# Kernel optimization log

Hardware: AMD Instinct MI355X
Metric: run time of the kernel (lower is better)

Reference implementation:

```python
import jax, jax.numpy as jnp
import numpy as np

D_MODEL = 320
N_CH = 129
N_TIMES = 200
D_STATE = 32
HEADDIM = 32
D_CONV = 4
N_LAYERS = 4
N_HEADS = 16
EPS = 1e-5


def _ln(x, w, b):
    m = jnp.mean(x, -1, keepdims=True)
    v = jnp.var(x, -1, keepdims=True)
    return (x - m) / jnp.sqrt(v + EPS) * w + b


def _mha(x, wqkv, bqkv, wo, bo, h):
    # torch nn.MultiheadAttention (batch_first, eval mode, avg attn weights)
    B, L, D = x.shape
    hd = D // h
    qkv = x @ wqkv.T + bqkv
    q, k, v = jnp.split(qkv, 3, axis=-1)
    sp = lambda t: t.reshape(B, L, h, hd).transpose(0, 2, 1, 3)
    q, k, v = sp(q), sp(k), sp(v)
    attn = jax.nn.softmax(jnp.einsum('bhqd,bhkd->bhqk', q, k) / np.sqrt(hd).astype(np.float32), axis=-1)
    o = jnp.einsum('bhqk,bhkd->bhqd', attn, v).transpose(0, 2, 1, 3).reshape(B, L, D)
    return o @ wo.T + bo, attn.mean(axis=1)


def _mamba2(u, in_w, conv_w, conv_b, dt_bias, A_log, Dskip, gn_w, out_w):
    # Mamba2 block, reference (non-fused) path, ngroups=1
    B, L, D = u.shape
    din = 2 * D
    H = din // HEADDIM
    P, N = HEADDIM, D_STATE
    zxbcdt = u @ in_w.T                       # (B,L,2*din+2N+H)
    z = zxbcdt[..., :din]
    xBC = zxbcdt[..., din:2 * din + 2 * N]
    dt = jax.nn.softplus(zxbcdt[..., -H:] + dt_bias)   # (B,L,H)
    # causal depthwise conv1d, kernel D_CONV, then silu
    xp = jnp.pad(xBC, ((0, 0), (D_CONV - 1, 0), (0, 0)))
    xc = conv_b + sum(xp[:, k:k + L, :] * conv_w[:, k] for k in range(D_CONV))
    xc = xc * jax.nn.sigmoid(xc)
    xh = xc[..., :din].reshape(B, L, H, P)
    Bm = xc[..., din:din + N]                 # (B,L,N)
    Cm = xc[..., din + N:]                    # (B,L,N)
    dA = jnp.exp(dt * (-jnp.exp(A_log)))      # (B,L,H)

    def step(st, inp):
        dA_t, dt_t, x_t, B_t, C_t = inp
        st = st * dA_t[:, :, None, None] + jnp.einsum('bh,bhp,bn->bhpn', dt_t, x_t, B_t)
        return st, jnp.einsum('bhpn,bn->bhp', st, C_t)

    mv = lambda t: jnp.moveaxis(t, 1, 0)
    st0 = jnp.zeros((B, H, P, N), u.dtype)
    _, ys = jax.lax.scan(step, st0, (mv(dA), mv(dt), mv(xh), mv(Bm), mv(Cm)))
    y = jnp.moveaxis(ys, 0, 1) + Dskip[None, None, :, None] * xh   # (B,L,H,P)
    y = y.reshape(B, L, din) * (z * jax.nn.sigmoid(z))             # gate
    y = y * jax.lax.rsqrt(jnp.mean(y * y, -1, keepdims=True) + EPS) * gn_w
    return y @ out_w.T


def _forward(x, sp_conv_w, sp_conv_b, sp_qkv_w, sp_qkv_b, sp_out_w, sp_out_b,
             sp_ln1_w, sp_ln1_b, sp_ff1_w, sp_ff1_b, sp_ff2_w, sp_ff2_b,
             sp_ln2_w, sp_ln2_b, norm_in_w, norm_in_b,
             m_in_w, m_conv_w, m_conv_b, m_dt_bias, m_A_log, m_D, m_gnorm_w, m_out_w,
             ln_w, ln_b, pm_qkv_w, pm_qkv_b, pm_out_w, pm_out_b, pm_ln_w, pm_ln_b,
             pool_w1, pool_b1, pool_w2, pool_b2, head_w1, head_b1, head_w2, head_b2):
    # spatial encoder: 1x1 conv projection -> MHA -> FFN
    h = jnp.einsum('bcl,dc->bld', x, sp_conv_w) + sp_conv_b        # (B,L,D)
    ha, sp_attn = _mha(h, sp_qkv_w, sp_qkv_b, sp_out_w, sp_out_b, N_HEADS)
    h = _ln(h + ha, sp_ln1_w, sp_ln1_b)
    ff = jax.nn.gelu(h @ sp_ff1_w.T + sp_ff1_b, approximate=False) @ sp_ff2_w.T + sp_ff2_b
    h = _ln(h + ff, sp_ln2_w, sp_ln2_b)
    h = _ln(h, norm_in_w, norm_in_b)
    # stacked pre-norm Mamba2 blocks with residuals
    for i in range(N_LAYERS):
        res = h
        h = _ln(h, ln_w[i], ln_b[i])
        h = _mamba2(h, m_in_w[i], m_conv_w[i], m_conv_b[i], m_dt_bias[i],
                    m_A_log[i], m_D[i], m_gnorm_w[i], m_out_w[i])
        h = h + res
    ha, post_attn = _mha(h, pm_qkv_w, pm_qkv_b, pm_out_w, pm_out_b, N_HEADS)
    h = _ln(h + ha, pm_ln_w, pm_ln_b)
    # attention-weighted pooling
    a = jnp.tanh(h @ pool_w1.T + pool_b1) @ pool_w2.T + pool_b2    # (B,L,1)
    a = jax.nn.softmax(a, axis=1)
    pooled = jnp.sum(h * a, axis=1)                                # (B,D)
    hr = jax.nn.gelu(pooled @ head_w1.T + head_b1, approximate=False)
    out = hr @ head_w2.T + head_b2                                 # (B,1)
    return out, sp_attn, post_attn, a.squeeze(-1)


def setup_inputs() -> dict:
    key = jax.random.key(0)
    ks = iter(jax.random.split(key, 64))
    nrm = lambda shape, s=0.02: jax.random.normal(next(ks), shape, jnp.float32) * s
    d, C, L, B = D_MODEL, N_CH, N_TIMES, 128
    din = 2 * d
    Hm = din // HEADDIM                       # 20 SSM heads
    dproj = 2 * din + 2 * D_STATE + Hm        # 1364
    cdim = din + 2 * D_STATE                  # 704
    nl = N_LAYERS
    return {
        'x': jax.random.normal(next(ks), (B, C, L), jnp.float32),
        'sp_conv_w': nrm((d, C)), 'sp_conv_b': jnp.zeros((d,), jnp.float32),
        'sp_qkv_w': nrm((3 * d, d)), 'sp_qkv_b': jnp.zeros((3 * d,), jnp.float32),
        'sp_out_w': nrm((d, d)), 'sp_out_b': jnp.zeros((d,), jnp.float32),
        'sp_ln1_w': jnp.ones((d,), jnp.float32), 'sp_ln1_b': jnp.zeros((d,), jnp.float32),
        'sp_ff1_w': nrm((2 * d, d)), 'sp_ff1_b': jnp.zeros((2 * d,), jnp.float32),
        'sp_ff2_w': nrm((d, 2 * d)), 'sp_ff2_b': jnp.zeros((d,), jnp.float32),
        'sp_ln2_w': jnp.ones((d,), jnp.float32), 'sp_ln2_b': jnp.zeros((d,), jnp.float32),
        'norm_in_w': jnp.ones((d,), jnp.float32), 'norm_in_b': jnp.zeros((d,), jnp.float32),
        'm_in_w': nrm((nl, dproj, d)),
        'm_conv_w': nrm((nl, cdim, D_CONV), 0.2),
        'm_conv_b': jnp.zeros((nl, cdim), jnp.float32),
        'm_dt_bias': jax.random.uniform(next(ks), (nl, Hm), jnp.float32, -0.1, 0.1),
        'm_A_log': jnp.log(jax.random.uniform(next(ks), (nl, Hm), jnp.float32, 1.0, 16.0)),
        'm_D': jnp.ones((nl, Hm), jnp.float32),
        'm_gnorm_w': jnp.ones((nl, din), jnp.float32),
        'm_out_w': nrm((nl, d, din)),
        'ln_w': jnp.ones((nl, d), jnp.float32), 'ln_b': jnp.zeros((nl, d), jnp.float32),
        'pm_qkv_w': nrm((3 * d, d)), 'pm_qkv_b': jnp.zeros((3 * d,), jnp.float32),
        'pm_out_w': nrm((d, d)), 'pm_out_b': jnp.zeros((d,), jnp.float32),
        'pm_ln_w': jnp.ones((d,), jnp.float32), 'pm_ln_b': jnp.zeros((d,), jnp.float32),
        'pool_w1': nrm((d // 4, d)), 'pool_b1': jnp.zeros((d // 4,), jnp.float32),
        'pool_w2': nrm((1, d // 4)), 'pool_b2': jnp.zeros((1,), jnp.float32),
        'head_w1': nrm((d // 2, d)), 'head_b1': jnp.zeros((d // 2,), jnp.float32),
        'head_w2': nrm((1, d // 2)), 'head_b2': jnp.zeros((1,), jnp.float32),
    }


def reference(x, sp_conv_w, sp_conv_b, sp_qkv_w, sp_qkv_b, sp_out_w, sp_out_b,
              sp_ln1_w, sp_ln1_b, sp_ff1_w, sp_ff1_b, sp_ff2_w, sp_ff2_b,
              sp_ln2_w, sp_ln2_b, norm_in_w, norm_in_b,
              m_in_w, m_conv_w, m_conv_b, m_dt_bias, m_A_log, m_D, m_gnorm_w, m_out_w,
              ln_w, ln_b, pm_qkv_w, pm_qkv_b, pm_out_w, pm_out_b, pm_ln_w, pm_ln_b,
              pool_w1, pool_b1, pool_w2, pool_b2, head_w1, head_b1, head_w2, head_b2):
    return _forward(x, sp_conv_w, sp_conv_b, sp_qkv_w, sp_qkv_b, sp_out_w, sp_out_b,
                    sp_ln1_w, sp_ln1_b, sp_ff1_w, sp_ff1_b, sp_ff2_w, sp_ff2_b,
                    sp_ln2_w, sp_ln2_b, norm_in_w, norm_in_b,
                    m_in_w, m_conv_w, m_conv_b, m_dt_bias, m_A_log, m_D, m_gnorm_w, m_out_w,
                    ln_w, ln_b, pm_qkv_w, pm_qkv_b, pm_out_w, pm_out_b, pm_ln_w, pm_ln_b,
                    pool_w1, pool_b1, pool_w2, pool_b2, head_w1, head_b1, head_w2, head_b2)
```

## Files before the change

kernel.cpp:

```cpp
#include <hip/hip_runtime.h>
#include <math.h>

#define BB 128
#define LL 200
#define DM 320
#define RTOT (BB*LL)
#define NCH 129
#define DIN 640
#define HM 20
#define PP 32
#define NN 32
#define CDIM 704
#define DPROJ 1364
#define NH 16
#define HD 20
#define ATTN_SCALE 0.22360679774997896f
#define KCONV 160

#define CH 32
#define NCHUNK 4
#define RC (CH*LL)

typedef unsigned short ushort;
typedef __attribute__((ext_vector_type(8))) short v8s;
typedef __attribute__((ext_vector_type(4))) float v4f;

static __device__ __forceinline__ float sigmoidf_(float x){ return 1.f/(1.f+__expf(-x)); }
static __device__ __forceinline__ float geluf_(float x){ return 0.5f*x*(1.f+erff(x*0.70710678118654752f)); }
static __device__ __forceinline__ ushort f2bf(float f){
  unsigned u = __float_as_uint(f);
  u = (u + 0x7FFFu + ((u>>16)&1u)) >> 16;
  return (ushort)u;
}
static __device__ __forceinline__ float bf2f(ushort h){ return __uint_as_float(((unsigned)h)<<16); }
static __device__ __forceinline__ void split3(float v, ushort* h, ushort* m, ushort* l){
  ushort hh = f2bf(v);
  float r1 = v - bf2f(hh);
  ushort mm = f2bf(r1);
  float r2 = r1 - bf2f(mm);
  *h = hh; *m = mm; *l = f2bf(r2);
}

static __device__ __forceinline__ float dpp_add_xor1(float v){
  return v + __int_as_float(__builtin_amdgcn_mov_dpp(__float_as_int(v), 0xB1, 0xF, 0xF, true));
}
static __device__ __forceinline__ float dpp_add_xor2(float v){
  return v + __int_as_float(__builtin_amdgcn_mov_dpp(__float_as_int(v), 0x4E, 0xF, 0xF, true));
}
static __device__ __forceinline__ float dpp_add_hm(float v){
  return v + __int_as_float(__builtin_amdgcn_mov_dpp(__float_as_int(v), 0x141, 0xF, 0xF, true));
}

#define GLL(g, s) __builtin_amdgcn_global_load_lds( \
    (const __attribute__((address_space(1))) unsigned int*)(g), \
    (__attribute__((address_space(3))) unsigned int*)(s), 16, 0, 0)

__global__ __launch_bounds__(256) void k_mgemm(
    const ushort* __restrict__ AH, const ushort* __restrict__ AM, const ushort* __restrict__ AL,
    const ushort* __restrict__ WH, const ushort* __restrict__ WM, const ushort* __restrict__ WL,
    const float* __restrict__ bias,
    float* __restrict__ outF, ushort* __restrict__ outH, ushort* __restrict__ outM, ushort* __restrict__ outL,
    int M, int N, int K, int lda, int act, int accum){
  __shared__ ushort sA0[128*32];
  __shared__ ushort sA1[128*32];
  __shared__ ushort sA2[128*32];
  __shared__ ushort sW0[128*32];
  __shared__ ushort sW1[128*32];
  __shared__ ushort sW2[128*32];
  int tid = threadIdx.x;
  int wid = tid>>6, lane = tid&63;
  int quad = lane>>4, col = lane&15;
  int m0 = blockIdx.y*128, n0 = blockIdx.x*128;
  int wm = (wid&1)*64, wn = (wid>>1)*64;
  v4f acc[4][4];
  #pragma unroll
  for (int i=0;i<4;i++)
    #pragma unroll
    for (int j=0;j<4;j++) acc[i][j] = (v4f)(0.f);

  int rl = lane>>2, kc8 = (lane&3)<<3;
  size_t aoff0 = (size_t)(m0 + 32*wid + rl)*lda + kc8;
  size_t aoff1 = aoff0 + (size_t)16*lda;
  int wr0 = n0 + 32*wid + rl;      if (wr0 > N-1) wr0 = N-1;
  int wr1 = n0 + 32*wid + 16 + rl; if (wr1 > N-1) wr1 = N-1;
  size_t woff0 = (size_t)wr0*K + kc8;
  size_t woff1 = (size_t)wr1*K + kc8;
  int sb0 = wid*1024, sb1 = wid*1024 + 512;

  for (int kb = 0; kb < K; kb += 32) {
    GLL(AH+aoff0+kb, &sA0[sb0]); GLL(AH+aoff1+kb, &sA0[sb1]);
    GLL(AM+aoff0+kb, &sA1[sb0]); GLL(AM+aoff1+kb, &sA1[sb1]);
    GLL(AL+aoff0+kb, &sA2[sb0]); GLL(AL+aoff1+kb, &sA2[sb1]);
    GLL(WH+woff0+kb, &sW0[sb0]); GLL(WH+woff1+kb, &sW0[sb1]);
    GLL(WM+woff0+kb, &sW1[sb0]); GLL(WM+woff1+kb, &sW1[sb1]);
    GLL(WL+woff0+kb, &sW2[sb0]); GLL(WL+woff1+kb, &sW2[sb1]);
    __syncthreads();
    v8s af[3][4];
    #pragma unroll
    for (int i=0;i<4;i++){
      int ro = (wm+16*i+col)*32 + quad*8;
      af[0][i] = *(const v8s*)&sA0[ro];
      af[1][i] = *(const v8s*)&sA1[ro];
      af[2][i] = *(const v8s*)&sA2[ro];
    }
    #pragma unroll
    for (int j=0;j<4;j++){
      int ro = (wn+16*j+col)*32 + quad*8;
      v8s b0 = *(const v8s*)&sW0[ro];
      v8s b1 = *(const v8s*)&sW1[ro];
      v8s b2 = *(const v8s*)&sW2[ro];
      #pragma unroll
      for (int i=0;i<4;i++){
        acc[i][j] = __builtin_amdgcn_mfma_f32_16x16x32_bf16(af[2][i], b0, acc[i][j], 0,0,0);
        acc[i][j] = __builtin_amdgcn_mfma_f32_16x16x32_bf16(af[1][i], b1, acc[i][j], 0,0,0);
        acc[i][j] = __builtin_amdgcn_mfma_f32_16x16x32_bf16(af[0][i], b2, acc[i][j], 0,0,0);
        acc[i][j] = __builtin_amdgcn_mfma_f32_16x16x32_bf16(af[1][i], b0, acc[i][j], 0,0,0);
        acc[i][j] = __builtin_amdgcn_mfma_f32_16x16x32_bf16(af[0][i], b1, acc[i][j], 0,0,0);
        acc[i][j] = __builtin_amdgcn_mfma_f32_16x16x32_bf16(af[0][i], b0, acc[i][j], 0,0,0);
      }
    }
    __syncthreads();
  }
  #pragma unroll
  for (int i=0;i<4;i++){
    int mb = m0 + wm + 16*i + quad*4;
    #pragma unroll
    for (int j=0;j<4;j++){
      int n = n0 + wn + 16*j + col;
      if (n >= N) continue;
      float bv = bias ? bias[n] : 0.f;
      #pragma unroll
      for (int r=0;r<4;r++){
        float v = acc[i][j][r] + bv;
        if (act == 1) v = geluf_(v);
        else if (act == 2) v = tanhf(v);
        size_t off = (size_t)(mb+r)*N + n;
        if (accum) v += outF[off];
        if (outF) outF[off] = v;
        if (outH) split3(v, outH+off, outM+off, outL+off);
      }
    }
  }
}

#define BM 128
#define BN 64
#define BKK 16
__global__ __launch_bounds__(256) void k_gemm(const float* __restrict__ A, const float* __restrict__ W,
    const float* __restrict__ bias, float* __restrict__ C, int M, int N, int K, int act, int accum){
  __shared__ float As[BKK][BM+4];
  __shared__ float Ws[BKK][BN+4];
  int tid = threadIdx.x;
  int m0 = blockIdx.y*BM, n0 = blockIdx.x*BN;
  int tx = tid & 15, ty = tid >> 4;
  float acc[8][4];
  #pragma unroll
  for (int i=0;i<8;i++)
    #pragma unroll
    for (int j=0;j<4;j++) acc[i][j]=0.f;
  for (int k0 = 0; k0 < K; k0 += BKK) {
    int r = tid >> 2, c4 = (tid & 3) << 2;
    #pragma unroll
    for (int hfl = 0; hfl < 2; hfl++) {
      int rr = r + hfl*64;
      float4 v = make_float4(0.f,0.f,0.f,0.f);
      if (m0 + rr < M && k0 + c4 < K)
        v = *(const float4*)(A + (size_t)(m0+rr)*K + k0 + c4);
      As[c4+0][rr]=v.x; As[c4+1][rr]=v.y; As[c4+2][rr]=v.z; As[c4+3][rr]=v.w;
    }
    {
      int n = tid >> 2;
      float4 v = make_float4(0.f,0.f,0.f,0.f);
      if (n0 + n < N && k0 + c4 < K)
        v = *(const float4*)(W + (size_t)(n0+n)*K + k0 + c4);
      Ws[c4+0][n]=v.x; Ws[c4+1][n]=v.y; Ws[c4+2][n]=v.z; Ws[c4+3][n]=v.w;
    }
    __syncthreads();
    #pragma unroll
    for (int kk = 0; kk < BKK; kk++) {
      float af[8], bf[4];
      float4 a0 = *(const float4*)&As[kk][ty*8];
      float4 a1 = *(const float4*)&As[kk][ty*8+4];
      af[0]=a0.x; af[1]=a0.y; af[2]=a0.z; af[3]=a0.w;
      af[4]=a1.x; af[5]=a1.y; af[6]=a1.z; af[7]=a1.w;
      float4 b0 = *(const float4*)&Ws[kk][tx*4];
      bf[0]=b0.x; bf[1]=b0.y; bf[2]=b0.z; bf[3]=b0.w;
      #pragma unroll
      for (int i=0;i<8;i++)
        #pragma unroll
        for (int j=0;j<4;j++) acc[i][j] = fmaf(af[i], bf[j], acc[i][j]);
    }
    __syncthreads();
  }
  #pragma unroll
  for (int i=0;i<8;i++){
    int m = m0 + ty*8 + i;
    if (m >= M) continue;
    #pragma unroll
    for (int j=0;j<4;j++){
      int n = n0 + tx*4 + j;
      if (n >= N) continue;
      float v = acc[i][j];
      if (bias) v += bias[n];
      if (act == 1) v = geluf_(v);
      else if (act == 2) v = tanhf(v);
      size_t off = (size_t)m*N + n;
      if (accum) v += C[off];
      C[off] = v;
    }
  }
}

__global__ __launch_bounds__(256) void k_wsplit(const float* __restrict__ src, ushort* __restrict__ hi,
    ushort* __restrict__ mi, ushort* __restrict__ lo, int N, int K, int Kp){
  int idx = blockIdx.x*256 + threadIdx.x;
  if (idx >= N*Kp) return;
  int n = idx / Kp, k = idx - n*Kp;
  float v = (k < K) ? src[(size_t)n*K + k] : 0.f;
  split3(v, hi+idx, mi+idx, lo+idx);
}

__global__ __launch_bounds__(256) void k_split(const float* __restrict__ src, ushort* __restrict__ hi,
    ushort* __restrict__ mi, ushort* __restrict__ lo, int n){
  int idx = blockIdx.x*256 + threadIdx.x;
  if (idx >= n) return;
  split3(src[idx], hi+idx, mi+idx, lo+idx);
}

__global__ __launch_bounds__(256) void k_tsplit(const float* __restrict__ x, ushort* __restrict__ hi,
    ushort* __restrict__ mi, ushort* __restrict__ lo, int r0g){
  int idx = blockIdx.x*256 + threadIdx.x;
  if (idx >= RC*KCONV) return;
  int r = idx / KCONV, c = idx - r*KCONV;
  int gr = r0g + r;
  int b = gr / LL, l = gr - b*LL;
  float v = (c < NCH) ? x[((size_t)b*NCH + c)*LL + l] : 0.f;
  split3(v, hi+idx, mi+idx, lo+idx);
}

__global__ __launch_bounds__(256) void k_ln(const float* __restrict__ A, const float* __restrict__ Badd,
    float* __restrict__ Of, ushort* __restrict__ Oh, ushort* __restrict__ Om, ushort* __restrict__ Ol,
    const float* __restrict__ w, const float* __restrict__ b, int nrows){
  int wid = threadIdx.x >> 6, lane = threadIdx.x & 63;
  int row = blockIdx.x*4 + wid;
  if (row >= nrows) return;
  const float* a = A + (size_t)row*DM;
  float x[5]; float s = 0.f;
  #pragma unroll
  for (int j=0;j<5;j++){
    int c = lane + j*64;
    x[j] = a[c];
    if (Badd) x[j] += Badd[(size_t)row*DM + c];
    s += x[j];
  }
  #pragma unroll
  for (int m=1;m<64;m<<=1) s += __shfl_xor(s, m);
  float mean = s * (1.f/DM);
  float vs = 0.f;
  #pragma unroll
  for (int j=0;j<5;j++){ float d = x[j]-mean; vs += d*d; }
  #pragma unroll
  for (int m=1;m<64;m<<=1) vs += __shfl_xor(vs, m);
  float inv = rsqrtf(vs*(1.f/DM) + 1e-5f);
  #pragma unroll
  for (int j=0;j<5;j++){
    int c = lane + j*64;
    float v = (x[j]-mean)*inv*w[c] + b[c];
    size_t off = (size_t)row*DM + c;
    if (Of) Of[off] = v;
    if (Oh) split3(v, Oh+off, Om+off, Ol+off);
  }
}

__global__ __launch_bounds__(256) void k_ln2x(const float* __restrict__ A, const float* __restrict__ F,
    const float* __restrict__ w2, const float* __restrict__ b2,
    const float* __restrict__ w3, const float* __restrict__ b3,
    float* __restrict__ O, int nrows){
  int wid = threadIdx.x >> 6, lane = threadIdx.x & 63;
  int row = blockIdx.x*4 + wid;
  if (row >= nrows) return;
  float x[5]; float s = 0.f;
  #pragma unroll
  for (int j=0;j<5;j++){
    int c = lane + j*64;
    x[j] = A[(size_t)row*DM + c] + F[(size_t)row*DM + c];
    s += x[j];
  }
  #pragma unroll
  for (int m=1;m<64;m<<=1) s += __shfl_xor(s, m);
  float mean = s * (1.f/DM);
  float vs = 0.f;
  #pragma unroll
  for (int j=0;j<5;j++){ float d = x[j]-mean; vs += d*d; }
  #pragma unroll
  for (int m=1;m<64;m<<=1) vs += __shfl_xor(vs, m);
  float inv = rsqrtf(vs*(1.f/DM) + 1e-5f);
  float s2 = 0.f;
  #pragma unroll
  for (int j=0;j<5;j++){
    int c = lane + j*64;
    x[j] = (x[j]-mean)*inv*w2[c] + b2[c];
    s2 += x[j];
  }
  #pragma unroll
  for (int m=1;m<64;m<<=1) s2 += __shfl_xor(s2, m);
  float mean2 = s2 * (1.f/DM);
  float vs2 = 0.f;
  #pragma unroll
  for (int j=0;j<5;j++){ float d = x[j]-mean2; vs2 += d*d; }
  #pragma unroll
  for (int m=1;m<64;m<<=1) vs2 += __shfl_xor(vs2, m);
  float inv2 = rsqrtf(vs2*(1.f/DM) + 1e-5f);
  #pragma unroll
  for (int j=0;j<5;j++){
    int c = lane + j*64;
    O[(size_t)row*DM + c] = (x[j]-mean2)*inv2*w3[c] + b3[c];
  }
}

__global__ __launch_bounds__(256) void k_attn1(const float* __restrict__ qkv,
    ushort* __restrict__ oh, ushort* __restrict__ om, ushort* __restrict__ ol, float* __restrict__ ml){
  __shared__ float Ks[LL*HD];
  __shared__ float Vs[LL*HD];
  int b = blockIdx.x >> 4, h = blockIdx.x & 15;
  int tid = threadIdx.x;
  for (int idx = tid; idx < LL*HD; idx += 256) {
    int r = idx / HD, c = idx - r*HD;
    const float* base = qkv + (size_t)(b*LL+r)*960 + h*HD + c;
    Ks[idx] = base[320];
    Vs[idx] = base[640];
  }
  __syncthreads();
  int q = tid;
  if (q >= LL) return;
  const float* qp = qkv + (size_t)(b*LL+q)*960 + h*HD;
  float qr[HD];
  #pragma unroll
  for (int d4 = 0; d4 < 5; d4++) {
    float4 v = *(const float4*)(qp + d4*4);
    qr[d4*4]=v.x; qr[d4*4+1]=v.y; qr[d4*4+2]=v.z; qr[d4*4+3]=v.w;
  }
  float m = -1e30f, l = 0.f;
  float o[HD];
  #pragma unroll
  for (int d=0; d<HD; d++) o[d]=0.f;
  for (int k = 0; k < LL; k++) {
    float s = 0.f;
    #pragma unroll
    for (int d = 0; d < HD; d++) s = fmaf(qr[d], Ks[k*HD+d], s);
    s *= ATTN_SCALE;
    float nm = fmaxf(m, s);
    float al = __expf(m - nm);
    float p  = __expf(s - nm);
    l = l*al + p;
    #pragma unroll
    for (int d = 0; d < HD; d++) o[d] = fmaf(p, Vs[k*HD+d], o[d]*al);
    m = nm;
  }
  float inv = 1.f/l;
  size_t ob = (size_t)(b*LL+q)*DM + h*HD;
  #pragma unroll
  for (int d = 0; d < HD; d++) {
    split3(o[d]*inv, oh+ob+d, om+ob+d, ol+ob+d);
  }
  size_t mlb = ((size_t)(b*NH+h)*LL + q)*2;
  ml[mlb+0] = m;
  ml[mlb+1] = l;
}

#define QS 164
__global__ __launch_bounds__(256) void k_attnmean(const float* __restrict__ qkv,
    const float* __restrict__ ml, float* __restrict__ outp){
  __shared__ float Qs[32*QS];
  __shared__ float Ksh[32*QS];
  __shared__ float Ms[NH*32];
  __shared__ float Ls[NH*32];
  int b = blockIdx.z;
  int q0 = blockIdx.y*32, k0 = blockIdx.x*32;
  int tid = threadIdx.x;
  for (int idx = tid; idx < NH*32; idx += 256) {
    int h = idx >> 5, r = idx & 31;
    int q = q0 + r;
    float m = 0.f, li = 1.f;
    if (q < LL) {
      size_t base = ((size_t)(b*NH+h)*LL + q)*2;
      m = ml[base+0];
      li = 1.f/ml[base+1];
    }
    Ms[idx] = m; Ls[idx] = li;
  }
  int tx = tid & 31, ty = tid >> 5;
  float acc[4] = {0.f,0.f,0.f,0.f};
  for (int hc = 0; hc < 2; hc++) {
    __syncthreads();
    for (int idx = tid; idx < 32*160; idx += 256) {
      int r = idx / 160, c = idx - r*160;
      int q = q0 + r, k = k0 + r;
      Qs[r*QS + c]  = (q < LL) ? qkv[(size_t)(b*LL+q)*960 + hc*160 + c] : 0.f;
      Ksh[r*QS + c] = (k < LL) ? qkv[(size_t)(b*LL+k)*960 + 320 + hc*160 + c] : 0.f;
    }
    __syncthreads();
    #pragma unroll
    for (int hh = 0; hh < 8; hh++) {
      int h = hc*8 + hh;
      float kf[HD];
      #pragma unroll
      for (int d4 = 0; d4 < 5; d4++) {
        float4 v = *(const float4*)&Ksh[tx*QS + hh*HD + d4*4];
        kf[d4*4]=v.x; kf[d4*4+1]=v.y; kf[d4*4+2]=v.z; kf[d4*4+3]=v.w;
      }
      #pragma unroll
      for (int j = 0; j < 4; j++) {
        int qr = ty + j*8;
        float s = 0.f;
        #pragma unroll
        for (int d4 = 0; d4 < 5; d4++) {
          float4 v = *(const float4*)&Qs[qr*QS + hh*HD + d4*4];
          s += v.x*kf[d4*4] + v.y*kf[d4*4+1] + v.z*kf[d4*4+2] + v.w*kf[d4*4+3];
        }
        acc[j] += __expf(s*ATTN_SCALE - Ms[h*32 + qr]) * Ls[h*32 + qr];
      }
    }
  }
  #pragma unroll
  for (int j = 0; j < 4; j++) {
    int q = q0 + ty + j*8, k = k0 + tx;
    if (q < LL && k < LL)
      outp[(size_t)(b*LL+q)*LL + k] = acc[j] * (1.f/NH);
  }
}

__global__ __launch_bounds__(256) void k_convBC(const float* __restrict__ big, const float* __restrict__ cw,
    const float* __restrict__ cb, float* __restrict__ xbc, int nrows){
  int idx = blockIdx.x*256 + threadIdx.x;
  if (idx >= nrows*64) return;
  int row = idx >> 6, j = idx & 63;
  int l = row % LL;
  int ch = 640 + j;
  float acc = cb[ch];
  #pragma unroll
  for (int k = 0; k < 4; k++) {
    int li = l - 3 + k;
    if (li >= 0) acc = fmaf(big[(size_t)(row-3+k)*DPROJ + 1280 + j], cw[ch*4+k], acc);
  }
  xbc[idx] = acc * sigmoidf_(acc);
}

__global__ __launch_bounds__(256) void k_scan(const float* __restrict__ big, const float* __restrict__ xbc,
    const float* __restrict__ cw, const float* __restrict__ cb,
    const float* __restrict__ dtb, const float* __restrict__ alog, const float* __restrict__ Dp,
    float* __restrict__ y){
  __shared__ float xs[LL*PP];
  __shared__ float2 dd[LL];
  int b = blockIdx.x / HM, h = blockIdx.x - (blockIdx.x/HM)*HM;
  int tid = threadIdx.x;
  for (int idx = tid; idx < LL*PP; idx += 256) {
    int r = idx >> 5, c = idx & 31;
    int ch = h*PP + c;
    float acc = cb[ch];
    #pragma unroll
    for (int k = 0; k < 4; k++) {
      int li = r - 3 + k;
      if (li >= 0) acc = fmaf(big[(size_t)(b*LL+li)*DPROJ + 640 + ch], cw[ch*4+k], acc);
    }
    xs[idx] = acc * sigmoidf_(acc);
  }
  float aexp = __expf(alog[h]);
  float dtbh = dtb[h];
  for (int idx = tid; idx < LL; idx += 256) {
    float raw = big[(size_t)(b*LL+idx)*DPROJ + 1344 + h] + dtbh;
    float sp = (raw > 30.f) ? raw : log1pf(__expf(raw));
    dd[idx] = make_float2(__expf(-aexp * sp), sp);
  }
  __syncthreads();
  int p = tid >> 3, ng = tid & 7, n0 = ng*4;
  float st0=0.f, st1=0.f, st2=0.f, st3=0.f;
  const float* base = xbc + (size_t)(b*LL)*64;
  float Dh = Dp[h];
  float4 Bc = *(const float4*)(base + n0);
  float4 Cc = *(const float4*)(base + 32 + n0);
  float  xv = xs[p];
  float2 ddc = dd[0];
  for (int t = 0; t < LL; t++) {
    float4 Bn = Bc, Cn = Cc;
    float  xn = xv;
    float2 ddn = ddc;
    if (t < LL-1) {
      Bn  = *(const float4*)(base + (size_t)(t+1)*64 + n0);
      Cn  = *(const float4*)(base + (size_t)(t+1)*64 + 32 + n0);
      xn  = xs[(t+1)*PP + p];
      ddn = dd[t+1];
    }
    float dav = ddc.x, dtv = ddc.y;
    float coef = dtv * xv;
    st0 = fmaf(coef, Bc.x, st0*dav);
    st1 = fmaf(coef, Bc.y, st1*dav);
    st2 = fmaf(coef, Bc.z, st2*dav);
    st3 = fmaf(coef, Bc.w, st3*dav);
    float part = st0*Cc.x + st1*Cc.y + st2*Cc.z + st3*Cc.w;
    part = dpp_add_xor1(part);
    part = dpp_add_xor2(part);
    part = dpp_add_hm(part);
    if (ng == 0) y[(size_t)(b*LL+t)*DIN + h*PP + p] = part + Dh*xv;
    Bc = Bn; Cc = Cn; xv = xn; ddc = ddn;
  }
}

__global__ __launch_bounds__(256) void k_mpost(const float* __restrict__ yc, float* __restrict__ big,
    const float* __restrict__ gw, int nrows){
  int wid = threadIdx.x >> 6, lane = threadIdx.x & 63;
  int row = blockIdx.x*4 + wid;
  if (row >= nrows) return;
  float v[10]; float ss = 0.f;
  #pragma unroll
  for (int j = 0; j < 10; j++) {
    int c = lane + j*64;
    float ys = yc[(size_t)row*DIN + c];
    float z  = big[(size_t)row*DPROJ + c];
    float val = ys * (z * sigmoidf_(z));
    v[j] = val; ss += val*val;
  }
  #pragma unroll
  for (int m=1;m<64;m<<=1) ss += __shfl_xor(ss, m);
  float scale = rsqrtf(ss*(1.f/DIN) + 1e-5f);
  ushort* rowp = (ushort*)(big + (size_t)row*DPROJ);
  #pragma unroll
  for (int j = 0; j < 10; j++) {
    int c = lane + j*64;
    float val = v[j]*scale*gw[c];
    split3(val, rowp+c, rowp+640+c, rowp+1280+c);
  }
}

__global__ __launch_bounds__(256) void k_pool2(const float* __restrict__ A, const float* __restrict__ w2,
    const float* __restrict__ b2, float* __restrict__ out, int nrows){
  int row = blockIdx.x*256 + threadIdx.x;
  if (row >= nrows) return;
  float s = b2[0];
  const float* a = A + (size_t)row*80;
  #pragma unroll
  for (int j = 0; j < 80; j++) s = fmaf(a[j], w2[j], s);
  out[row] = s;
}

__global__ __launch_bounds__(256) void k_pool(const float* __restrict__ logits, const float* __restrict__ h,
    float* __restrict__ a_out, float* __restrict__ pooled){
  __shared__ float red[256];
  __shared__ float as_[LL];
  int b = blockIdx.x, tid = threadIdx.x;
  float v = (tid < LL) ? logits[b*LL + tid] : -1e30f;
  red[tid] = v; __syncthreads();
  for (int s=128; s>0; s>>=1){ if (tid<s) red[tid]=fmaxf(red[tid],red[tid+s]); __syncthreads(); }
  float mx = red[0]; __syncthreads();
  float e = (tid<LL) ? __expf(v - mx) : 0.f;
  red[tid] = e; __syncthreads();
  for (int s=128; s>0; s>>=1){ if (tid<s) red[tid]+=red[tid+s]; __syncthreads(); }
  float inv = 1.f/red[0];
  if (tid < LL){ float av = e*inv; as_[tid]=av; a_out[b*LL+tid]=av; }
  __syncthreads();
  for (int d = tid; d < DM; d += 256) {
    float s = 0.f;
    for (int l=0;l<LL;l++) s = fmaf(h[(size_t)(b*LL+l)*DM + d], as_[l], s);
    pooled[b*DM + d] = s;
  }
}

__global__ __launch_bounds__(128) void k_head2(const float* __restrict__ hr, const float* __restrict__ w2,
    const float* __restrict__ b2, float* __restrict__ out){
  int b = threadIdx.x;
  if (b >= BB) return;
  float s = b2[0];
  const float* a = hr + (size_t)b*160;
  #pragma unroll
  for (int j = 0; j < 160; j++) s = fmaf(a[j], w2[j], s);
  out[b] = s;
}

static inline void mgemm(const ushort* AH, const ushort* AM, const ushort* AL,
    const ushort* WH, const ushort* WM, const ushort* WL,
    const float* bias, float* outF, ushort* outH, ushort* outM, ushort* outL,
    int M, int N, int K, int lda, int act, int accum, hipStream_t s){
  hipLaunchKernelGGL(k_mgemm, dim3((N+127)/128, M/128), dim3(256), 0, s,
                     AH, AM, AL, WH, WM, WL, bias, outF, outH, outM, outL, M, N, K, lda, act, accum);
}
static inline void wsplit(const float* src, ushort* hi, ushort* mi, ushort* lo, int N, int K, int Kp, hipStream_t s){
  hipLaunchKernelGGL(k_wsplit, dim3((N*Kp+255)/256), dim3(256), 0, s, src, hi, mi, lo, N, K, Kp);
}

#define F_WCONVH ((size_t)8192000)
#define F_WCONVM ((size_t)8217600)
#define F_WCONVL ((size_t)8243200)
#define F_WQKVH  ((size_t)8268800)
#define F_WQKVM  ((size_t)8422400)
#define F_WQKVL  ((size_t)8576000)
#define F_WOUTH  ((size_t)8729600)
#define F_WOUTM  ((size_t)8780800)
#define F_WOUTL  ((size_t)8832000)
#define F_WFF1H  ((size_t)8883200)
#define F_WFF1M  ((size_t)8985600)
#define F_WFF1L  ((size_t)9088000)
#define F_WFF2H  ((size_t)9190400)
#define F_WFF2M  ((size_t)9292800)
#define F_WFF2L  ((size_t)9395200)
#define F_WINH   ((size_t)9497600)
#define F_WINM   ((size_t)10370560)
#define F_WINL   ((size_t)11243520)
#define F_WMOH   ((size_t)12116480)
#define F_WMOM   ((size_t)12526080)
#define F_WMOL   ((size_t)12935680)
#define F_WPQH   ((size_t)13345280)
#define F_WPQM   ((size_t)13498880)
#define F_WPQL   ((size_t)13652480)
#define F_WPOH   ((size_t)13806080)
#define F_WPOM   ((size_t)13857280)
#define F_WPOL   ((size_t)13908480)
#define F_WPLH   ((size_t)13959680)
#define F_WPLM   ((size_t)13972480)
#define F_WPLL   ((size_t)13985280)
#define SB       ((size_t)13998080)
#define S_XTH  (SB+0)
#define S_XTM  (SB+512000)
#define S_XTL  (SB+1024000)
#define S_HH   (SB+1536000)
#define S_HM   (SB+2560000)
#define S_HL   (SB+3584000)
#define S_TH   (SB+4608000)
#define S_TM   (SB+5632000)
#define S_TL   (SB+6656000)
#define S_QKV  (SB+7680000)
#define S_FF1H (SB+7680000)
#define S_FF1M (SB+9728000)
#define S_FF1L (SB+11776000)
#define S_P1   (SB+7680000)
#define S_ML   (SB+13824000)
#define S_DEST (SB+14028800)
#define S_LOG  (SB+16076800)
#define S_PL   (SB+16102400)
#define S_HR   (SB+16143360)
#define B_MTH  (SB+0)
#define B_MTM  (SB+1024000)
#define B_MTL  (SB+2048000)
#define B_BIG  (SB+3072000)
#define B_XBC  (SB+0)
#define B_YC   (SB+11801600)

#define O_OUT ((size_t)0)
#define O_A1  ((size_t)128)
#define O_A2  ((size_t)5120128)
#define O_A   ((size_t)10240128)

extern "C" void kernel_launch(void* const* d_in, const int* in_sizes, int n_in,
                              void* d_out, int out_size, void* d_ws, size_t ws_size,
                              hipStream_t stream) {
  const float* x         = (const float*)d_in[0];
  const float* sp_conv_w = (const float*)d_in[1];
  const float* sp_conv_b = (const float*)d_in[2];
  const float* sp_qkv_w  = (const float*)d_in[3];
  const float* sp_qkv_b  = (const float*)d_in[4];
  const float* sp_out_w  = (const float*)d_in[5];
  const float* sp_out_b  = (const float*)d_in[6];
  const float* sp_ln1_w  = (const float*)d_in[7];
  const float* sp_ln1_b  = (const float*)d_in[8];
  const float* sp_ff1_w  = (const float*)d_in[9];
  const float* sp_ff1_b  = (const float*)d_in[10];
  const float* sp_ff2_w  = (const float*)d_in[11];
  const float* sp_ff2_b  = (const float*)d_in[12];
  const float* sp_ln2_w  = (const float*)d_in[13];
  const float* sp_ln2_b  = (const float*)d_in[14];
  const float* norm_in_w = (const float*)d_in[15];
  const float* norm_in_b = (const float*)d_in[16];
  const float* m_in_w    = (const float*)d_in[17];
  const float* m_conv_w  = (const float*)d_in[18];
  const float* m_conv_b  = (const float*)d_in[19];
  const float* m_dt_bias = (const float*)d_in[20];
  const float* m_A_log   = (const float*)d_in[21];
  const float* m_D       = (const float*)d_in[22];
  const float* m_gnorm_w = (const float*)d_in[23];
  const float* m_out_w   = (const float*)d_in[24];
  const float* ln_w      = (const float*)d_in[25];
  const float* ln_b      = (const float*)d_in[26];
  const float* pm_qkv_w  = (const float*)d_in[27];
  const float* pm_qkv_b  = (const float*)d_in[28];
  const float* pm_out_w  = (const float*)d_in[29];
  const float* pm_out_b  = (const float*)d_in[30];
  const float* pm_ln_w   = (const float*)d_in[31];
  const float* pm_ln_b   = (const float*)d_in[32];
  const float* pool_w1   = (const float*)d_in[33];
  const float* pool_b1   = (const float*)d_in[34];
  const float* pool_w2   = (const float*)d_in[35];
  const float* pool_b2   = (const float*)d_in[36];
  const float* head_w1   = (const float*)d_in[37];
  const float* head_b1   = (const float*)d_in[38];
  const float* head_w2   = (const float*)d_in[39];
  const float* head_b2   = (const float*)d_in[40];

  float* ws  = (float*)d_ws;
  float* H   = ws;
  float* out = (float*)d_out;

  #define U(off) ((ushort*)(ws + (off)))

  wsplit(sp_conv_w, U(F_WCONVH), U(F_WCONVM), U(F_WCONVL), DM, NCH, KCONV, stream);
  wsplit(sp_qkv_w,  U(F_WQKVH),  U(F_WQKVM),  U(F_WQKVL),  3*DM, DM, DM, stream);
  wsplit(sp_out_w,  U(F_WOUTH),  U(F_WOUTM),  U(F_WOUTL),  DM, DM, DM, stream);
  wsplit(sp_ff1_w,  U(F_WFF1H),  U(F_WFF1M),  U(F_WFF1L),  DIN, DM, DM, stream);
  wsplit(sp_ff2_w,  U(F_WFF2H),  U(F_WFF2M),  U(F_WFF2L),  DM, DIN, DIN, stream);
  for (int i = 0; i < 4; i++) {
    size_t wo = (size_t)i*DPROJ*DM;
    wsplit(m_in_w + wo, U(F_WINH)+wo, U(F_WINM)+wo, U(F_WINL)+wo, DPROJ, DM, DM, stream);
    size_t wo2 = (size_t)i*DM*DIN;
    wsplit(m_out_w + wo2, U(F_WMOH)+wo2, U(F_WMOM)+wo2, U(F_WMOL)+wo2, DM, DIN, DIN, stream);
  }
  wsplit(pm_qkv_w, U(F_WPQH), U(F_WPQM), U(F_WPQL), 3*DM, DM, DM, stream);
  wsplit(pm_out_w, U(F_WPOH), U(F_WPOM), U(F_WPOL), DM, DM, DM, stream);
  wsplit(pool_w1,  U(F_WPLH), U(F_WPLM), U(F_WPLL), 80, DM, DM, stream);

  for (int c = 0; c < NCHUNK; c++) {
    float* Hc = H + (size_t)c*RC*DM;
    hipLaunchKernelGGL(k_tsplit, dim3((RC*KCONV+255)/256), dim3(256), 0, stream, x,
                       U(S_XTH), U(S_XTM), U(S_XTL), c*RC);
    mgemm(U(S_XTH), U(S_XTM), U(S_XTL), U(F_WCONVH), U(F_WCONVM), U(F_WCONVL), sp_conv_b,
          Hc, U(S_HH), U(S_HM), U(S_HL), RC, DM, KCONV, KCONV, 0, 0, stream);
    mgemm(U(S_HH), U(S_HM), U(S_HL), U(F_WQKVH), U(F_WQKVM), U(F_WQKVL), sp_qkv_b,
          ws + S_QKV, nullptr, nullptr, nullptr, RC, 3*DM, DM, DM, 0, 0, stream);
    hipLaunchKernelGGL(k_attn1, dim3(CH*NH), dim3(256), 0, stream, ws + S_QKV,
                       U(S_TH), U(S_TM), U(S_TL), ws + S_ML);
    hipLaunchKernelGGL(k_attnmean, dim3(7,7,CH), dim3(256), 0, stream, ws + S_QKV,
                       ws + S_ML, out + O_A1 + (size_t)c*RC*LL);
    mgemm(U(S_TH), U(S_TM), U(S_TL), U(F_WOUTH), U(F_WOUTM), U(F_WOUTL), sp_out_b,
          ws + S_DEST, nullptr, nullptr, nullptr, RC, DM, DM, DM, 0, 0, stream);
    hipLaunchKernelGGL(k_ln, dim3(RC/4), dim3(256), 0, stream, Hc, ws + S_DEST,
                       Hc, U(S_HH), U(S_HM), U(S_HL), sp_ln1_w, sp_ln1_b, RC);
    mgemm(U(S_HH), U(S_HM), U(S_HL), U(F_WFF1H), U(F_WFF1M), U(F_WFF1L), sp_ff1_b,
          nullptr, U(S_FF1H), U(S_FF1M), U(S_FF1L), RC, DIN, DM, DM, 1, 0, stream);
    mgemm(U(S_FF1H), U(S_FF1M), U(S_FF1L), U(F_WFF2H), U(F_WFF2M), U(F_WFF2L), sp_ff2_b,
          ws + S_DEST, nullptr, nullptr, nullptr, RC, DM, DIN, DIN, 0, 0, stream);
    hipLaunchKernelGGL(k_ln2x, dim3(RC/4), dim3(256), 0, stream, Hc, ws + S_DEST,
                       sp_ln2_w, sp_ln2_b, norm_in_w, norm_in_b, Hc, RC);
  }

  for (int i = 0; i < 4; i++) {
    const ushort* WIH = U(F_WINH) + (size_t)i*DPROJ*DM;
    const ushort* WIM = U(F_WINM) + (size_t)i*DPROJ*DM;
    const ushort* WIL = U(F_WINL) + (size_t)i*DPROJ*DM;
    const ushort* WOH = U(F_WMOH) + (size_t)i*DM*DIN;
    const ushort* WOM = U(F_WMOM) + (size_t)i*DM*DIN;
    const ushort* WOL = U(F_WMOL) + (size_t)i*DM*DIN;
    const float* cwi = m_conv_w + (size_t)i*CDIM*4;
    const float* cbi = m_conv_b + (size_t)i*CDIM;
    for (int c = 0; c < NCHUNK; c++) {
      float* Hc = H + (size_t)c*RC*DM;
      float* BIG = ws + B_BIG;
      hipLaunchKernelGGL(k_ln, dim3(RC/4), dim3(256), 0, stream, Hc, (const float*)nullptr,
                         (float*)nullptr, U(B_MTH), U(B_MTM), U(B_MTL),
                         ln_w + (size_t)i*DM, ln_b + (size_t)i*DM, RC);
      mgemm(U(B_MTH), U(B_MTM), U(B_MTL), WIH, WIM, WIL, nullptr,
            BIG, nullptr, nullptr, nullptr, RC, DPROJ, DM, DM, 0, 0, stream);
      hipLaunchKernelGGL(k_convBC, dim3((RC*64+255)/256), dim3(256), 0, stream, BIG,
                         cwi, cbi, ws + B_XBC, RC);
      hipLaunchKernelGGL(k_scan, dim3(CH*HM), dim3(256), 0, stream, BIG, ws + B_XBC,
                         cwi, cbi, m_dt_bias + (size_t)i*HM, m_A_log + (size_t)i*HM,
                         m_D + (size_t)i*HM, ws + B_YC);
      hipLaunchKernelGGL(k_mpost, dim3(RC/4), dim3(256), 0, stream, ws + B_YC, BIG,
                         m_gnorm_w + (size_t)i*DIN, RC);
      mgemm((const ushort*)BIG, (const ushort*)BIG + 640, (const ushort*)BIG + 1280,
            WOH, WOM, WOL, nullptr, Hc, nullptr, nullptr, nullptr,
            RC, DM, DIN, DPROJ*2, 0, 1, stream);
    }
  }

  for (int c = 0; c < NCHUNK; c++) {
    float* Hc = H + (size_t)c*RC*DM;
    hipLaunchKernelGGL(k_split, dim3((RC*DM+255)/256), dim3(256), 0, stream, Hc,
                       U(S_HH), U(S_HM), U(S_HL), RC*DM);
    mgemm(U(S_HH), U(S_HM), U(S_HL), U(F_WPQH), U(F_WPQM), U(F_WPQL), pm_qkv_b,
          ws + S_QKV, nullptr, nullptr, nullptr, RC, 3*DM, DM, DM, 0, 0, stream);
    hipLaunchKernelGGL(k_attn1, dim3(CH*NH), dim3(256), 0, stream, ws + S_QKV,
                       U(S_TH), U(S_TM), U(S_TL), ws + S_ML);
    hipLaunchKernelGGL(k_attnmean, dim3(7,7,CH), dim3(256), 0, stream, ws + S_QKV,
                       ws + S_ML, out + O_A2 + (size_t)c*RC*LL);
    mgemm(U(S_TH), U(S_TM), U(S_TL), U(F_WPOH), U(F_WPOM), U(F_WPOL), pm_out_b,
          ws + S_DEST, nullptr, nullptr, nullptr, RC, DM, DM, DM, 0, 0, stream);
    hipLaunchKernelGGL(k_ln, dim3(RC/4), dim3(256), 0, stream, Hc, ws + S_DEST,
                       Hc, U(S_HH), U(S_HM), U(S_HL), pm_ln_w, pm_ln_b, RC);
    mgemm(U(S_HH), U(S_HM), U(S_HL), U(F_WPLH), U(F_WPLM), U(F_WPLL), pool_b1,
          ws + S_P1, nullptr, nullptr, nullptr, RC, 80, DM, DM, 2, 0, stream);
    hipLaunchKernelGGL(k_pool2, dim3((RC+255)/256), dim3(256), 0, stream, ws + S_P1, pool_w2, pool_b2,
                       ws + S_LOG + (size_t)c*RC, RC);
  }

  hipLaunchKernelGGL(k_pool, dim3(BB), dim3(256), 0, stream, ws + S_LOG, H, out + O_A, ws + S_PL);
  hipLaunchKernelGGL(k_gemm, dim3((160+BN-1)/BN, (BB+BM-1)/BM), dim3(256), 0, stream,
                     ws + S_PL, head_w1, head_b1, ws + S_HR, BB, 160, DM, 1, 0);
  hipLaunchKernelGGL(k_head2, dim3(1), dim3(128), 0, stream, ws + S_HR, head_w2, head_b2, out + O_OUT);
}
```

Before: 7.108 ms.

## Fuse B/C conv into scan kernel and stage scan in two LDS halves

Removes the separate k_convBC launch. Each scan block now computes the causal conv plus SiLU for the B/C channels itself and keeps the results in shared memory. The time axis is processed in two halves of 100 steps so that x, B and C fit in LDS. Scan outputs are written back into the x buffer and then stored coalesced to y. In exchange, the B/C conv is recomputed redundantly by each of the 20 head blocks per batch, and extra syncs are added between the halves.

New measurement: 6.474 ms. 8.9% less time.

```diff
diff --git a/kernel.cpp b/kernel.cpp
--- a/kernel.cpp
+++ b/kernel.cpp
@@ -430,41 +430,16 @@
   }
 }
 
-__global__ __launch_bounds__(256) void k_convBC(const float* __restrict__ big, const float* __restrict__ cw,
-    const float* __restrict__ cb, float* __restrict__ xbc, int nrows){
-  int idx = blockIdx.x*256 + threadIdx.x;
-  if (idx >= nrows*64) return;
-  int row = idx >> 6, j = idx & 63;
-  int l = row % LL;
-  int ch = 640 + j;
-  float acc = cb[ch];
-  #pragma unroll
-  for (int k = 0; k < 4; k++) {
-    int li = l - 3 + k;
-    if (li >= 0) acc = fmaf(big[(size_t)(row-3+k)*DPROJ + 1280 + j], cw[ch*4+k], acc);
-  }
-  xbc[idx] = acc * sigmoidf_(acc);
-}
-
-__global__ __launch_bounds__(256) void k_scan(const float* __restrict__ big, const float* __restrict__ xbc,
+#define HT 100
+__global__ __launch_bounds__(256) void k_scan(const float* __restrict__ big,
     const float* __restrict__ cw, const float* __restrict__ cb,
     const float* __restrict__ dtb, const float* __restrict__ alog, const float* __restrict__ Dp,
     float* __restrict__ y){
-  __shared__ float xs[LL*PP];
+  __shared__ float xs[HT*PP];
+  __shared__ float bc[HT*64];
   __shared__ float2 dd[LL];
   int b = blockIdx.x / HM, h = blockIdx.x - (blockIdx.x/HM)*HM;
   int tid = threadIdx.x;
-  for (int idx = tid; idx < LL*PP; idx += 256) {
-    int r = idx >> 5, c = idx & 31;
-    int ch = h*PP + c;
-    float acc = cb[ch];
-    #pragma unroll
-    for (int k = 0; k < 4; k++) {
-      int li = r - 3 + k;
-      if (li >= 0) acc = fmaf(big[(size_t)(b*LL+li)*DPROJ + 640 + ch], cw[ch*4+k], acc);
-    }
-    xs[idx] = acc * sigmoidf_(acc);
-  }
   float aexp = __expf(alog[h]);
   float dtbh = dtb[h];
   for (int idx = tid; idx < LL; idx += 256) {
@@ -472,37 +447,69 @@
     float sp = (raw > 30.f) ? raw : log1pf(__expf(raw));
     dd[idx] = make_float2(__expf(-aexp * sp), sp);
   }
-  __syncthreads();
   int p = tid >> 3, ng = tid & 7, n0 = ng*4;
   float st0=0.f, st1=0.f, st2=0.f, st3=0.f;
-  const float* base = xbc + (size_t)(b*LL)*64;
   float Dh = Dp[h];
-  float4 Bc = *(const float4*)(base + n0);
-  float4 Cc = *(const float4*)(base + 32 + n0);
-  float  xv = xs[p];
-  float2 ddc = dd[0];
-  for (int t = 0; t < LL; t++) {
-    float4 Bn = Bc, Cn = Cc;
-    float  xn = xv;
-    float2 ddn = ddc;
-    if (t < LL-1) {
-      Bn  = *(const float4*)(base + (size_t)(t+1)*64 + n0);
-      Cn  = *(const float4*)(base + (size_t)(t+1)*64 + 32 + n0);
-      xn  = xs[(t+1)*PP + p];
-      ddn = dd[t+1];
-    }
-    float dav = ddc.x, dtv = ddc.y;
-    float coef = dtv * xv;
-    st0 = fmaf(coef, Bc.x, st0*dav);
-    st1 = fmaf(coef, Bc.y, st1*dav);
-    st2 = fmaf(coef, Bc.z, st2*dav);
-    st3 = fmaf(coef, Bc.w, st3*dav);
-    float part = st0*Cc.x + st1*Cc.y + st2*Cc.z + st3*Cc.w;
-    part = dpp_add_xor1(part);
-    part = dpp_add_xor2(part);
-    part = dpp_add_hm(part);
-    if (ng == 0) y[(size_t)(b*LL+t)*DIN + h*PP + p] = part + Dh*xv;
-    Bc = Bn; Cc = Cn; xv = xn; ddc = ddn;
+  for (int half = 0; half < 2; half++) {
+    int t0 = half*HT;
+    __syncthreads();
+    for (int idx = tid; idx < HT*PP; idx += 256) {
+      int r = idx >> 5, c = idx & 31;
+      int gr = t0 + r;
+      int ch = h*PP + c;
+      float acc = cb[ch];
+      #pragma unroll
+      for (int k = 0; k < 4; k++) {
+        int li = gr - 3 + k;
+        if (li >= 0) acc = fmaf(big[(size_t)(b*LL+li)*DPROJ + 640 + ch], cw[ch*4+k], acc);
+      }
+      xs[idx] = acc * sigmoidf_(acc);
+    }
+    for (int idx = tid; idx < HT*64; idx += 256) {
+      int r = idx >> 6, j = idx & 63;
+      int gr = t0 + r;
+      int ch = 640 + j;
+      float acc = cb[ch];
+      #pragma unroll
+      for (int k = 0; k < 4; k++) {
+        int li = gr - 3 + k;
+        if (li >= 0) acc = fmaf(big[(size_t)(b*LL+li)*DPROJ + 1280 + j], cw[ch*4+k], acc);
+      }
+      bc[idx] = acc * sigmoidf_(acc);
+    }
+    __syncthreads();
+    float4 Bc = *(const float4*)&bc[n0];
+    float4 Cc = *(const float4*)&bc[32 + n0];
+    float  xv = xs[p];
+    float2 ddc = dd[t0];
+    for (int tt = 0; tt < HT; tt++) {
+      float4 Bn = Bc, Cn = Cc;
+      float  xn = xv;
+      float2 ddn = ddc;
+      if (tt < HT-1) {
+        Bn  = *(const float4*)&bc[(tt+1)*64 + n0];
+        Cn  = *(const float4*)&bc[(tt+1)*64 + 32 + n0];
+        xn  = xs[(tt+1)*PP + p];
+        ddn = dd[t0+tt+1];
+      }
+      float dav = ddc.x, dtv = ddc.y;
+      float coef = dtv * xv;
+      st0 = fmaf(coef, Bc.x, st0*dav);
+      st1 = fmaf(coef, Bc.y, st1*dav);
+      st2 = fmaf(coef, Bc.z, st2*dav);
+      st3 = fmaf(coef, Bc.w, st3*dav);
+      float part = st0*Cc.x + st1*Cc.y + st2*Cc.z + st3*Cc.w;
+      part = dpp_add_xor1(part);
+      part = dpp_add_xor2(part);
+      part = dpp_add_hm(part);
+      if (ng == 0) xs[tt*PP + p] = part + Dh*xv;
+      Bc = Bn; Cc = Cn; xv = xn; ddc = ddn;
+    }
+    __syncthreads();
+    for (int idx = tid; idx < HT*PP; idx += 256) {
+      int r = idx >> 5, c = idx & 31;
+      y[(size_t)(b*LL + t0 + r)*DIN + h*PP + c] = xs[idx];
+    }
   }
 }
 
@@ -641,7 +648,6 @@
 #define B_MTM  (SB+1024000)
 #define B_MTL  (SB+2048000)
 #define B_BIG  (SB+3072000)
-#define B_XBC  (SB+0)
 #define B_YC   (SB+11801600)
 
 #define O_OUT ((size_t)0)
@@ -756,9 +762,7 @@
                          ln_w + (size_t)i*DM, ln_b + (size_t)i*DM, RC);
       mgemm(U(B_MTH), U(B_MTM), U(B_MTL), WIH, WIM, WIL, nullptr,
             BIG, nullptr, nullptr, nullptr, RC, DPROJ, DM, DM, 0, 0, stream);
-      hipLaunchKernelGGL(k_convBC, dim3((RC*64+255)/256), dim3(256), 0, stream, BIG,
-                         cwi, cbi, ws + B_XBC, RC);
-      hipLaunchKernelGGL(k_scan, dim3(CH*HM), dim3(256), 0, stream, BIG, ws + B_XBC,
+      hipLaunchKernelGGL(k_scan, dim3(CH*HM), dim3(256), 0, stream, BIG,
                          cwi, cbi, m_dt_bias + (size_t)i*HM, m_A_log + (size_t)i*HM,
                          m_D + (size_t)i*HM, ws + B_YC);
       hipLaunchKernelGGL(k_mpost, dim3(RC/4), dim3(256), 0, stream, ws + B_YC, BIG,
```
